# Kernel tuning notes

Measured on AMD Instinct MI355X. Metric: run time of the kernel, lower is better.

Reference implementation:

```python
import jax, jax.numpy as jnp
import numpy as np

LOG2 = float(np.log(2.0))

def ssp(x):
    # shifted softplus used throughout SchNet
    return jax.nn.softplus(x) - LOG2

def setup_inputs() -> dict:
    key = jax.random.key(0)
    ks = jax.random.split(key, 12)
    B, Na, Nn, G, F = 16, 512, 64, 25, 128
    s = 0.05
    return {
        "x": jax.random.normal(ks[0], (B, Na, F), jnp.float32),
        "r_ij": jax.random.uniform(ks[1], (B, Na, Nn), jnp.float32),
        "f_ij": jax.random.uniform(ks[2], (B, Na, Nn, G), jnp.float32),
        "neighbours": jax.random.randint(ks[3], (B, Na, Nn), 0, Na),
        "pairwise_mask": jax.random.uniform(ks[4], (B, Na, Nn), jnp.float32),
        "W_in2f": jax.random.normal(ks[5], (F, F), jnp.float32) * s,
        "W_f1": jax.random.normal(ks[6], (G, F), jnp.float32) * s,
        "b_f1": jnp.zeros((F,), jnp.float32),
        "W_f2": jax.random.normal(ks[7], (F, F), jnp.float32) * s,
        "b_f2": jnp.zeros((F,), jnp.float32),
        "W_out": jax.random.normal(ks[8], (F, F), jnp.float32) * s,
        "b_out": jnp.zeros((F,), jnp.float32),
    }

def reference(x, r_ij, f_ij, neighbours, pairwise_mask,
              W_in2f, W_f1, b_f1, W_f2, b_f2, W_out, b_out):
    # filter_network: Dense(G->F, ssp) -> Dense(F->F)
    W = jnp.einsum('bang,gf->banf', f_ij, W_f1) + b_f1  # [B,Na,Nn,F]
    W = ssp(W)
    W = jnp.einsum('banf,fg->bang', W, W_f2) + b_f2
    # in2f (no bias)
    y = jnp.einsum('bai,if->baf', x, W_in2f)  # [B,Na,F]
    B, Na, Nn = neighbours.shape
    # gather neighbor features: y[b, neighbours[b,a,n], :]
    nbh = neighbours.reshape(B, Na * Nn, 1)
    g = jnp.take_along_axis(y, nbh, axis=1).reshape(B, Na, Nn, -1)
    # filter multiply, mask, aggregate over neighbor axis (sum, no mean)
    agg = jnp.sum(g * W * pairwise_mask[..., None], axis=2)  # [B,Na,F]
    # f2out with shifted softplus activation
    out = ssp(jnp.einsum('baf,fo->bao', agg, W_out) + b_out)
    return out
```

## Files before the change

kernel.cpp:

```cpp
#include <hip/hip_runtime.h>

typedef __attribute__((ext_vector_type(8))) short bf16x8;
typedef __attribute__((ext_vector_type(4))) float f32x4;
typedef __attribute__((ext_vector_type(4))) unsigned int u32x4;

#define LOG2F 0.69314718055994531f
#define LOG2EF 1.4426950408889634f

#define NB 16
#define NA 512
#define NN 64
#define NG 25
#define NF 128

__device__ __forceinline__ unsigned short f2bf(float x) {
    __bf16 h = (__bf16)x;
    return __builtin_bit_cast(unsigned short, h);
}
__device__ __forceinline__ float ssp2(float s) {
    float t = __builtin_amdgcn_exp2f(s);
    return fmaf(__builtin_amdgcn_logf(1.0f + t), LOG2F, -LOG2F);
}

#define FRAG_WF1 0
#define FRAG_WF2 4096
#define FRAG_WIN 20480
#define FRAG_WOUT 36864
#define B1S_OFF   106496
#define YBF_OFF   107008
#define AGG_OFF   2204160

__global__ __launch_bounds__(256) void k_prep(
    const float* __restrict__ Wf1, const float* __restrict__ Wf2,
    const float* __restrict__ Win, const float* __restrict__ Wout,
    const float* __restrict__ b1, char* __restrict__ ws)
{
    unsigned short* frag = (unsigned short*)ws;
    int idx = blockIdx.x * 256 + threadIdx.x;
    if (idx < 4096) {
        int j = idx & 7, lane = (idx >> 3) & 63, tc = idx >> 9;
        int f1 = tc * 16 + (lane & 15);
        int g  = (lane >> 4) * 8 + j;
        frag[idx] = (g < NG) ? f2bf(Wf1[g * NF + f1] * LOG2EF) : (unsigned short)0;
    } else if (idx < 20480) {
        int t = idx - 4096;
        int j = t & 7, lane = (t >> 3) & 63, ks = (t >> 9) & 3, tn = t >> 11;
        int f = tn * 16 + (lane & 15);
        int k = ks * 32 + (lane >> 4) * 8 + j;
        frag[idx] = f2bf(Wf2[k * NF + f]);
    } else if (idx < 36864) {
        int t = idx - 20480;
        int j = t & 7, lane = (t >> 3) & 63, ks = (t >> 9) & 3, tn = t >> 11;
        int f = tn * 16 + (lane & 15);
        int k = ks * 32 + (lane >> 4) * 8 + j;
        frag[idx] = f2bf(Win[k * NF + f]);
    } else if (idx < 53248) {
        int t = idx - 36864;
        int j = t & 7, lane = (t >> 3) & 63, ks = (t >> 9) & 3, tn = t >> 11;
        int f = tn * 16 + (lane & 15);
        int k = ks * 32 + (lane >> 4) * 8 + j;
        frag[idx] = f2bf(Wout[k * NF + f]);
    } else if (idx < 53376) {
        ((float*)(ws + B1S_OFF))[idx - 53248] = b1[idx - 53248] * LOG2EF;
    }
}

__global__ __launch_bounds__(256) void k_in2f(
    const float* __restrict__ x, const unsigned short* __restrict__ frag,
    unsigned short* __restrict__ ybf)
{
    const unsigned short* winfrag = frag + FRAG_WIN;
    const int lane = threadIdx.x & 63, w = threadIdx.x >> 6;
    const int rowbase = blockIdx.x * 32;
    f32x4 acc[2][2];
    f32x4 z = {0.f, 0.f, 0.f, 0.f};
    acc[0][0] = z; acc[0][1] = z; acc[1][0] = z; acc[1][1] = z;
#pragma unroll
    for (int ks = 0; ks < 4; ++ks) {
        bf16x8 a[2];
#pragma unroll
        for (int tm = 0; tm < 2; ++tm) {
            int row = rowbase + tm * 16 + (lane & 15);
            int k0  = ks * 32 + (lane >> 4) * 8;
            const float* p = x + (size_t)row * NF + k0;
            float4 v0 = *(const float4*)p;
            float4 v1 = *(const float4*)(p + 4);
            bf16x8 t;
            t[0] = (short)f2bf(v0.x); t[1] = (short)f2bf(v0.y);
            t[2] = (short)f2bf(v0.z); t[3] = (short)f2bf(v0.w);
            t[4] = (short)f2bf(v1.x); t[5] = (short)f2bf(v1.y);
            t[6] = (short)f2bf(v1.z); t[7] = (short)f2bf(v1.w);
            a[tm] = t;
        }
#pragma unroll
        for (int tn = 0; tn < 2; ++tn) {
            bf16x8 bfr = *(const bf16x8*)(winfrag + ((((w * 2 + tn) * 4 + ks) * 64) + lane) * 8);
#pragma unroll
            for (int tm = 0; tm < 2; ++tm)
                acc[tm][tn] = __builtin_amdgcn_mfma_f32_16x16x32_bf16(a[tm], bfr, acc[tm][tn], 0, 0, 0);
        }
    }
#pragma unroll
    for (int tm = 0; tm < 2; ++tm)
#pragma unroll
        for (int tn = 0; tn < 2; ++tn)
#pragma unroll
            for (int r = 0; r < 4; ++r) {
                int row = rowbase + tm * 16 + (lane >> 4) * 4 + r;
                int idx = (lane & 15) * 8 + w * 2 + tn;
                ybf[(size_t)row * NF + idx] = f2bf(acc[tm][tn][r]);
            }
}

__global__ __launch_bounds__(256, 4) void k_cfconv(
    const float* __restrict__ fij, const int* __restrict__ nbh,
    const float* __restrict__ mask, const float* __restrict__ b1s,
    const float* __restrict__ b2, const unsigned short* __restrict__ frag,
    const unsigned short* __restrict__ ybf, float* __restrict__ agg)
{
    __shared__ alignas(16) char smem[16896];
    float* sfij          = (float*)smem;
    unsigned short* sW1T = (unsigned short*)smem;
    float* smask         = (float*)(smem + 16384);
    int*   snbh          = (int*)(smem + 16640);

    const int tid = threadIdx.x, lane = tid & 63, w = tid >> 6;
    const int g = lane >> 4, lc = lane & 15;
    const int atom = blockIdx.x;
    const int bidx = atom >> 9;

    if (tid < 64) {
        smask[tid] = mask[(size_t)atom * NN + tid];
        snbh[tid]  = nbh[(size_t)atom * NN + tid];
    }

    {
        const char* fb = (const char*)(fij + (size_t)atom * (NN * NG));
        __builtin_amdgcn_global_load_lds(
            (const __attribute__((address_space(1))) void*)(fb + w * 1024 + lane * 16),
            (__attribute__((address_space(3))) void*)((char*)sfij + w * 1024), 16, 0, 0);
        if (w < 2) {
            __builtin_amdgcn_global_load_lds(
                (const __attribute__((address_space(1))) void*)(fb + (w + 4) * 1024 + lane * 16),
                (__attribute__((address_space(3))) void*)((char*)sfij + (w + 4) * 1024), 16, 0, 0);
        }
        if (w == 3) {
            __builtin_amdgcn_global_load_lds(
                (const __attribute__((address_space(1))) void*)(fb + 6144 + lane * 4),
                (__attribute__((address_space(3))) void*)((char*)sfij + 6144), 4, 0, 0);
        }
    }

    const unsigned short* wf1frag = frag + FRAG_WF1;
    bf16x8 afr[2], bfr[4];
#pragma unroll
    for (int i = 0; i < 2; ++i)
        afr[i] = *(const bf16x8*)(wf1frag + (((2 * w + i) * 64) + lane) * 8);

    __syncthreads();

    {
        const int g0 = g * 8;
        const unsigned int m0 = (g == 3) ? 0x0000FFFFu : 0xFFFFFFFFu;
        const unsigned int m1 = (g == 3) ? 0u : 0xFFFFFFFFu;
#pragma unroll
        for (int tn = 0; tn < 4; ++tn) {
            int n = tn * 16 + lc;
            const float* p = sfij + n * NG + g0;
            bf16x8 t;
            t[0] = (short)f2bf(p[0]); t[1] = (short)f2bf(p[1]);
            t[2] = (short)f2bf(p[2]); t[3] = (short)f2bf(p[3]);
            t[4] = (short)f2bf(p[4]); t[5] = (short)f2bf(p[5]);
            t[6] = (short)f2bf(p[6]); t[7] = (short)f2bf(p[7]);
            u32x4 tv = __builtin_bit_cast(u32x4, t);
            tv[0] &= m0; tv[1] &= m1; tv[2] &= m1; tv[3] &= m1;
            bfr[tn] = __builtin_bit_cast(bf16x8, tv);
        }
    }

    __syncthreads();

    f32x4 dW[2][4];
#pragma unroll
    for (int i = 0; i < 2; ++i) {
        int c0 = (2 * w + i) * 16 + g * 4;
        f32x4 ci = *(const f32x4*)(b1s + c0);
#pragma unroll
        for (int tn = 0; tn < 4; ++tn)
            dW[i][tn] = __builtin_amdgcn_mfma_f32_16x16x32_bf16(afr[i], bfr[tn], ci, 0, 0, 0);
    }

#pragma unroll
    for (int i = 0; i < 2; ++i) {
        int c0 = (2 * w + i) * 16 + g * 4;
#pragma unroll
        for (int tn = 0; tn < 4; ++tn) {
            int n = tn * 16 + lc;
            ushort4 pk;
#pragma unroll
            for (int r = 0; r < 4; ++r)
                ((unsigned short*)&pk)[r] = f2bf(ssp2(dW[i][tn][r]));
            *(ushort4*)((char*)sW1T + n * 256 + ((c0 * 2) ^ ((n & 7) << 4))) = pk;
        }
    }
    __syncthreads();

    const unsigned short* wf2frag = frag + FRAG_WF2;
    const int fbase = w * 32;
    const int fc0 = fbase + lc;
    const float bias0 = b2[fc0], bias1 = b2[fc0 + 16];
    f32x4 acc[4][2];
#pragma unroll
    for (int tm = 0; tm < 4; ++tm) {
        acc[tm][0] = f32x4{bias0, bias0, bias0, bias0};
        acc[tm][1] = f32x4{bias1, bias1, bias1, bias1};
    }
#pragma unroll
    for (int ks = 0; ks < 4; ++ks) {
        bf16x8 a4[4];
#pragma unroll
        for (int tm = 0; tm < 4; ++tm) {
            int n  = tm * 16 + lc;
            int kb = ks * 64 + g * 16;
            a4[tm] = *(const bf16x8*)((char*)sW1T + n * 256 + (kb ^ ((n & 7) << 4)));
        }
#pragma unroll
        for (int tnl = 0; tnl < 2; ++tnl) {
            int tn = w * 2 + tnl;
            bf16x8 bf2 = *(const bf16x8*)(wf2frag + (((tn * 4 + ks) * 64) + lane) * 8);
#pragma unroll
            for (int tm = 0; tm < 4; ++tm)
                acc[tm][tnl] = __builtin_amdgcn_mfma_f32_16x16x32_bf16(a4[tm], bf2, acc[tm][tnl], 0, 0, 0);
        }
    }

    float aggv0 = 0.f, aggv1 = 0.f;
    const unsigned short* yb = ybf + (size_t)bidx * NA * NF;
    const int ycol = lc * 8 + 2 * w;
#pragma unroll
    for (int tm = 0; tm < 4; ++tm) {
        f32x4 m4 = *(const f32x4*)(smask + tm * 16 + g * 4);
        int4  nb4 = *(const int4*)(snbh + tm * 16 + g * 4);
#pragma unroll
        for (int r = 0; r < 4; ++r) {
            int yrow = (r == 0) ? nb4.x : (r == 1) ? nb4.y : (r == 2) ? nb4.z : nb4.w;
            unsigned int u = *(const unsigned int*)(yb + (size_t)yrow * NF + ycol);
            float y0 = __builtin_bit_cast(float, u << 16);
            float y1 = __builtin_bit_cast(float, u & 0xFFFF0000u);
            aggv0 = fmaf(acc[tm][0][r] * m4[r], y0, aggv0);
            aggv1 = fmaf(acc[tm][1][r] * m4[r], y1, aggv1);
        }
    }
    aggv0 += __shfl_xor(aggv0, 16); aggv1 += __shfl_xor(aggv1, 16);
    aggv0 += __shfl_xor(aggv0, 32); aggv1 += __shfl_xor(aggv1, 32);
    if (lane < 16) {
        float* ap = agg + (size_t)atom * NF + fbase;
        ap[lane] = aggv0;
        ap[16 + lane] = aggv1;
    }
}

__global__ __launch_bounds__(256) void k_out(
    const float* __restrict__ agg, const unsigned short* __restrict__ frag,
    const float* __restrict__ bout, float* __restrict__ out)
{
    const unsigned short* wofrag = frag + FRAG_WOUT;
    const int lane = threadIdx.x & 63, w = threadIdx.x >> 6;
    const int rowbase = blockIdx.x * 32;
    const int f0 = w * 32 + (lane & 15);
    const float bo0 = bout[f0], bo1 = bout[f0 + 16];
    f32x4 acc[2][2];
    acc[0][0] = f32x4{bo0, bo0, bo0, bo0};
    acc[1][0] = f32x4{bo0, bo0, bo0, bo0};
    acc[0][1] = f32x4{bo1, bo1, bo1, bo1};
    acc[1][1] = f32x4{bo1, bo1, bo1, bo1};
#pragma unroll
    for (int ks = 0; ks < 4; ++ks) {
        bf16x8 a[2];
#pragma unroll
        for (int tm = 0; tm < 2; ++tm) {
            int row = rowbase + tm * 16 + (lane & 15);
            int k0  = ks * 32 + (lane >> 4) * 8;
            const float* p = agg + (size_t)row * NF + k0;
            float4 v0 = *(const float4*)p;
            float4 v1 = *(const float4*)(p + 4);
            bf16x8 t;
            t[0] = (short)f2bf(v0.x); t[1] = (short)f2bf(v0.y);
            t[2] = (short)f2bf(v0.z); t[3] = (short)f2bf(v0.w);
            t[4] = (short)f2bf(v1.x); t[5] = (short)f2bf(v1.y);
            t[6] = (short)f2bf(v1.z); t[7] = (short)f2bf(v1.w);
            a[tm] = t;
        }
#pragma unroll
        for (int tn = 0; tn < 2; ++tn) {
            bf16x8 bfr = *(const bf16x8*)(wofrag + ((((w * 2 + tn) * 4 + ks) * 64) + lane) * 8);
#pragma unroll
            for (int tm = 0; tm < 2; ++tm)
                acc[tm][tn] = __builtin_amdgcn_mfma_f32_16x16x32_bf16(a[tm], bfr, acc[tm][tn], 0, 0, 0);
        }
    }
    float lg2 = LOG2EF;
#pragma unroll
    for (int tm = 0; tm < 2; ++tm)
#pragma unroll
        for (int tn = 0; tn < 2; ++tn)
#pragma unroll
            for (int r = 0; r < 4; ++r) {
                int row = rowbase + tm * 16 + (lane >> 4) * 4 + r;
                int f   = w * 32 + tn * 16 + (lane & 15);
                out[(size_t)row * NF + f] = ssp2(acc[tm][tn][r] * lg2);
            }
}

extern "C" void kernel_launch(void* const* d_in, const int* in_sizes, int n_in,
                              void* d_out, int out_size, void* d_ws, size_t ws_size,
                              hipStream_t stream)
{
    (void)in_sizes; (void)n_in; (void)out_size; (void)ws_size;
    const float* x    = (const float*)d_in[0];
    const float* fij  = (const float*)d_in[2];
    const int*   nbh  = (const int*)d_in[3];
    const float* mask = (const float*)d_in[4];
    const float* Win  = (const float*)d_in[5];
    const float* Wf1  = (const float*)d_in[6];
    const float* b1   = (const float*)d_in[7];
    const float* Wf2  = (const float*)d_in[8];
    const float* b2   = (const float*)d_in[9];
    const float* Wout = (const float*)d_in[10];
    const float* bout = (const float*)d_in[11];
    float* out = (float*)d_out;

    char* ws = (char*)d_ws;
    unsigned short* frag = (unsigned short*)ws;
    const float*    b1s  = (const float*)(ws + B1S_OFF);
    unsigned short* ybf  = (unsigned short*)(ws + YBF_OFF);
    float*          agg  = (float*)(ws + AGG_OFF);

    k_prep  <<<209,  256, 0, stream>>>(Wf1, Wf2, Win, Wout, b1, ws);
    k_in2f  <<<256,  256, 0, stream>>>(x, frag, ybf);
    k_cfconv<<<8192, 256, 0, stream>>>(fij, nbh, mask, b1s, b2, frag, ybf, agg);
    k_out   <<<256,  256, 0, stream>>>(agg, frag, bout, out);
}
```

Baseline: 70.91 us.

## Reuse registers across cfconv stages, raise occupancy bound, use natural y layout

The cfconv kernel now shares one register array between the first-layer filter accumulators and the second-layer accumulators, and reuses the B-fragment array for the LDS A-loads. This cuts live registers so the launch bound can rise from 4 to 6 waves-per-SIMD hint. The in2f kernel now writes y in natural feature order, so the gather does two 16-bit loads per neighbour instead of one packed 32-bit load. That trades fewer, wider gather loads for extra occupancy and more in-flight gathers.

```diff
diff --git a/kernel.cpp b/kernel.cpp
--- a/kernel.cpp
+++ b/kernel.cpp
@@ -107,12 +107,12 @@
 #pragma unroll
             for (int r = 0; r < 4; ++r) {
                 int row = rowbase + tm * 16 + (lane >> 4) * 4 + r;
-                int idx = (lane & 15) * 8 + w * 2 + tn;
-                ybf[(size_t)row * NF + idx] = f2bf(acc[tm][tn][r]);
+                int f   = w * 32 + tn * 16 + (lane & 15);
+                ybf[(size_t)row * NF + f] = f2bf(acc[tm][tn][r]);
             }
 }
 
-__global__ __launch_bounds__(256, 4) void k_cfconv(
+__global__ __launch_bounds__(256, 6) void k_cfconv(
     const float* __restrict__ fij, const int* __restrict__ nbh,
     const float* __restrict__ mask, const float* __restrict__ b1s,
     const float* __restrict__ b2, const unsigned short* __restrict__ frag,
@@ -128,6 +128,8 @@
     const int g = lane >> 4, lc = lane & 15;
     const int atom = blockIdx.x;
     const int bidx = atom >> 9;
+    const int fbase = w * 32;
+    const int fc0 = fbase + lc;
 
     if (tid < 64) {
         smask[tid] = mask[(size_t)atom * NN + tid];
@@ -152,7 +154,8 @@
     }
 
     const unsigned short* wf1frag = frag + FRAG_WF1;
-    bf16x8 afr[2], bfr[4];
+    bf16x8 afr[2], vb[4];
+    f32x4  rg[8];
 #pragma unroll
     for (int i = 0; i < 2; ++i)
         afr[i] = *(const bf16x8*)(wf1frag + (((2 * w + i) * 64) + lane) * 8);
@@ -174,20 +177,19 @@
             t[6] = (short)f2bf(p[6]); t[7] = (short)f2bf(p[7]);
             u32x4 tv = __builtin_bit_cast(u32x4, t);
             tv[0] &= m0; tv[1] &= m1; tv[2] &= m1; tv[3] &= m1;
-            bfr[tn] = __builtin_bit_cast(bf16x8, tv);
+            vb[tn] = __builtin_bit_cast(bf16x8, tv);
         }
     }
 
     __syncthreads();
 
-    f32x4 dW[2][4];
 #pragma unroll
     for (int i = 0; i < 2; ++i) {
         int c0 = (2 * w + i) * 16 + g * 4;
         f32x4 ci = *(const f32x4*)(b1s + c0);
 #pragma unroll
         for (int tn = 0; tn < 4; ++tn)
-            dW[i][tn] = __builtin_amdgcn_mfma_f32_16x16x32_bf16(afr[i], bfr[tn], ci, 0, 0, 0);
+            rg[i * 4 + tn] = __builtin_amdgcn_mfma_f32_16x16x32_bf16(afr[i], vb[tn], ci, 0, 0, 0);
     }
 
 #pragma unroll
@@ -199,30 +201,26 @@
             ushort4 pk;
 #pragma unroll
             for (int r = 0; r < 4; ++r)
-                ((unsigned short*)&pk)[r] = f2bf(ssp2(dW[i][tn][r]));
+                ((unsigned short*)&pk)[r] = f2bf(ssp2(rg[i * 4 + tn][r]));
             *(ushort4*)((char*)sW1T + n * 256 + ((c0 * 2) ^ ((n & 7) << 4))) = pk;
         }
     }
     __syncthreads();
 
     const unsigned short* wf2frag = frag + FRAG_WF2;
-    const int fbase = w * 32;
-    const int fc0 = fbase + lc;
     const float bias0 = b2[fc0], bias1 = b2[fc0 + 16];
-    f32x4 acc[4][2];
 #pragma unroll
     for (int tm = 0; tm < 4; ++tm) {
-        acc[tm][0] = f32x4{bias0, bias0, bias0, bias0};
-        acc[tm][1] = f32x4{bias1, bias1, bias1, bias1};
+        rg[tm * 2 + 0] = f32x4{bias0, bias0, bias0, bias0};
+        rg[tm * 2 + 1] = f32x4{bias1, bias1, bias1, bias1};
     }
 #pragma unroll
     for (int ks = 0; ks < 4; ++ks) {
-        bf16x8 a4[4];
 #pragma unroll
         for (int tm = 0; tm < 4; ++tm) {
             int n  = tm * 16 + lc;
             int kb = ks * 64 + g * 16;
-            a4[tm] = *(const bf16x8*)((char*)sW1T + n * 256 + (kb ^ ((n & 7) << 4)));
+            vb[tm] = *(const bf16x8*)((char*)sW1T + n * 256 + (kb ^ ((n & 7) << 4)));
         }
 #pragma unroll
         for (int tnl = 0; tnl < 2; ++tnl) {
@@ -230,13 +228,12 @@
             bf16x8 bf2 = *(const bf16x8*)(wf2frag + (((tn * 4 + ks) * 64) + lane) * 8);
 #pragma unroll
             for (int tm = 0; tm < 4; ++tm)
-                acc[tm][tnl] = __builtin_amdgcn_mfma_f32_16x16x32_bf16(a4[tm], bf2, acc[tm][tnl], 0, 0, 0);
+                rg[tm * 2 + tnl] = __builtin_amdgcn_mfma_f32_16x16x32_bf16(vb[tm], bf2, rg[tm * 2 + tnl], 0, 0, 0);
         }
     }
 
     float aggv0 = 0.f, aggv1 = 0.f;
     const unsigned short* yb = ybf + (size_t)bidx * NA * NF;
-    const int ycol = lc * 8 + 2 * w;
 #pragma unroll
     for (int tm = 0; tm < 4; ++tm) {
         f32x4 m4 = *(const f32x4*)(smask + tm * 16 + g * 4);
@@ -244,11 +241,11 @@
 #pragma unroll
         for (int r = 0; r < 4; ++r) {
             int yrow = (r == 0) ? nb4.x : (r == 1) ? nb4.y : (r == 2) ? nb4.z : nb4.w;
-            unsigned int u = *(const unsigned int*)(yb + (size_t)yrow * NF + ycol);
-            float y0 = __builtin_bit_cast(float, u << 16);
-            float y1 = __builtin_bit_cast(float, u & 0xFFFF0000u);
-            aggv0 = fmaf(acc[tm][0][r] * m4[r], y0, aggv0);
-            aggv1 = fmaf(acc[tm][1][r] * m4[r], y1, aggv1);
+            const unsigned short* yp = yb + (size_t)yrow * NF + fc0;
+            float y0 = __builtin_bit_cast(float, (unsigned int)yp[0] << 16);
+            float y1 = __builtin_bit_cast(float, (unsigned int)yp[16] << 16);
+            aggv0 = fmaf(rg[tm * 2 + 0][r] * m4[r], y0, aggv0);
+            aggv1 = fmaf(rg[tm * 2 + 1][r] * m4[r], y1, aggv1);
         }
     }
     aggv0 += __shfl_xor(aggv0, 16); aggv1 += __shfl_xor(aggv1, 16);
```

Result: faster. 59.38 us (-16.3%).
